# Kernel tuning notes

Measured on AMD Instinct MI355X. Metric: run time of the kernel, lower is better.

Reference implementation:

```python
import jax, jax.numpy as jnp
import numpy as np

H = 16      # num_heads
D = 1024    # input_dim
F = 4096    # feed_forward_hidden_size
B, S = 8, 4096
EPS = 1e-6


def _ln(x, g, b):
    mu = jnp.mean(x, axis=-1, keepdims=True)
    var = jnp.mean(jnp.square(x - mu), axis=-1, keepdims=True)
    return (x - mu) * jax.lax.rsqrt(var + EPS) * g + b


def _attn(Q, K, V):
    # per-head attention; original scales by sqrt(input_dim), NOT sqrt(head_dim)
    b, sq, d = Q.shape
    sk = K.shape[1]
    dh = d // H
    Qh = Q.reshape(b, sq, H, dh)
    Kh = K.reshape(b, sk, H, dh)
    Vh = V.reshape(b, sk, H, dh)
    scores = jnp.einsum('bqhd,bkhd->bhqk', Qh, Kh) / jnp.sqrt(jnp.float32(d))
    w = jax.nn.softmax(scores, axis=-1)
    return jnp.einsum('bhqk,bkhd->bqhd', w, Vh).reshape(b, sq, d)


def setup_inputs() -> dict:
    key = jax.random.key(0)
    ks = jax.random.split(key, 10)
    sc = 0.02
    np.random.seed(42)
    decode_input = jnp.asarray(np.random.random([B, 1, D]).astype(np.float32))
    return {
        'key': jax.random.normal(ks[0], (B, S, D), jnp.float32),
        'value': jax.random.normal(ks[1], (B, S, D), jnp.float32),
        'decode_input': decode_input,
        'Wq': jax.random.normal(ks[2], (D, D), jnp.float32) * sc,
        'bq': jnp.zeros((D,), jnp.float32),
        'Wk': jax.random.normal(ks[3], (D, D), jnp.float32) * sc,
        'bk': jnp.zeros((D,), jnp.float32),
        'Wv': jax.random.normal(ks[4], (D, D), jnp.float32) * sc,
        'bv': jnp.zeros((D,), jnp.float32),
        'Wo': jax.random.normal(ks[5], (D, D), jnp.float32) * sc,
        'bo': jnp.zeros((D,), jnp.float32),
        'W1': jax.random.normal(ks[6], (D, F), jnp.float32) * sc,
        'b1': jnp.zeros((F,), jnp.float32),
        'W2': jax.random.normal(ks[7], (F, D), jnp.float32) * sc,
        'b2': jnp.zeros((D,), jnp.float32),
        'ln2_g': jnp.ones((D,), jnp.float32),
        'ln2_b': jnp.zeros((D,), jnp.float32),
        'lnf_g': jnp.ones((D,), jnp.float32),
        'lnf_b': jnp.zeros((D,), jnp.float32),
    }


def reference(key, value, decode_input, Wq, bq, Wk, bk, Wv, bv, Wo, bo,
              W1, b1, W2, b2, ln2_g, ln2_b, lnf_g, lnf_b):
    # K/V projections shared by both attention calls (original reuses mha_1)
    K = key @ Wk + bk            # [B,S,D]
    V = value @ Wv + bv          # [B,S,D]

    # mha_1: self-attention of decode_input would use its own K/V, but here
    # q=k=v=decode_input for the first call
    Q1 = decode_input @ Wq + bq
    K1 = decode_input @ Wk + bk
    V1 = decode_input @ Wv + bv
    mha1_out = _attn(Q1, K1, V1) @ Wo + bo   # [B,1,D]
    # note: layer_norm_mha_1 output is computed in original but never used

    # second call (original buggily calls mha_1 again): q=mha1_out (un-normed)
    Q2 = mha1_out @ Wq + bq
    mha2_out = _attn(Q2, K, V) @ Wo + bo     # [B,1,D]
    x = _ln(mha2_out + decode_input, ln2_g, ln2_b)

    ff = jax.nn.relu(x @ W1 + b1) @ W2 + b2
    return _ln(ff + x, lnf_g, lnf_b)
```

## Files before the change

### kernel.cpp

```cpp
#include <hip/hip_runtime.h>
#include <hip/hip_bf16.h>

#define NB 8
#define NS 4096
#define ND 1024
#define NH 16
#define NF 4096

typedef __attribute__((ext_vector_type(8))) short s16x8;
typedef __attribute__((ext_vector_type(4))) float f32x4;

__device__ __forceinline__ short f2bfs(float x) {
    __hip_bfloat16 h = __float2bfloat16(x);
    return *reinterpret_cast<short*>(&h);
}

__device__ __forceinline__ s16x8 pack8(float4 a, float4 b) {
    s16x8 r;
    r[0]=f2bfs(a.x); r[1]=f2bfs(a.y); r[2]=f2bfs(a.z); r[3]=f2bfs(a.w);
    r[4]=f2bfs(b.x); r[5]=f2bfs(b.y); r[6]=f2bfs(b.z); r[7]=f2bfs(b.w);
    return r;
}

template<int KC>
__global__ void __launch_bounds__(256) mvV_k(const float* __restrict__ x,
        const float* __restrict__ W, int K, int Cout, float* __restrict__ Pout)
{
    __shared__ float xs[KC * 8];
    int tid = threadIdx.x;
    int c = blockIdx.x * 256 + tid;
    int k0 = blockIdx.y * KC;
    for (int i = tid; i < KC * 8; i += 256) {
        int k = i >> 3, b = i & 7;
        xs[i] = x[(size_t)b * K + k0 + k];
    }
    __syncthreads();
    const float* Wp = W + (size_t)k0 * Cout + c;
    float acc[8] = {0,0,0,0,0,0,0,0};
    #pragma unroll 16
    for (int k = 0; k < KC; ++k) {
        float wv = Wp[(size_t)k * Cout];
        float4 x0 = *(const float4*)&xs[k * 8];
        float4 x1 = *(const float4*)&xs[k * 8 + 4];
        acc[0] += x0.x * wv; acc[1] += x0.y * wv; acc[2] += x0.z * wv; acc[3] += x0.w * wv;
        acc[4] += x1.x * wv; acc[5] += x1.y * wv; acc[6] += x1.z * wv; acc[7] += x1.w * wv;
    }
    float* op = Pout + ((size_t)blockIdx.y * 8) * Cout + c;
    #pragma unroll
    for (int b = 0; b < 8; ++b) op[(size_t)b * Cout] = acc[b];
}

template<int KC, int NP, int RELU>
__global__ void __launch_bounds__(256) mvP_k(const float* __restrict__ P,
        const float* __restrict__ bias, const float* __restrict__ W,
        int K, int Cout, float* __restrict__ Pout)
{
    __shared__ float xs[KC * 8];
    int tid = threadIdx.x;
    int c = blockIdx.x * 256 + tid;
    int k0 = blockIdx.y * KC;
    for (int i = tid; i < KC * 8; i += 256) {
        int b = i / KC, k = i % KC;
        float t = bias[k0 + k];
        #pragma unroll 8
        for (int p = 0; p < NP; ++p) t += P[((size_t)(p * 8 + b)) * K + k0 + k];
        if (RELU) t = fmaxf(t, 0.f);
        xs[k * 8 + b] = t;
    }
    __syncthreads();
    const float* Wp = W + (size_t)k0 * Cout + c;
    float acc[8] = {0,0,0,0,0,0,0,0};
    #pragma unroll 16
    for (int k = 0; k < KC; ++k) {
        float wv = Wp[(size_t)k * Cout];
        float4 x0 = *(const float4*)&xs[k * 8];
        float4 x1 = *(const float4*)&xs[k * 8 + 4];
        acc[0] += x0.x * wv; acc[1] += x0.y * wv; acc[2] += x0.z * wv; acc[3] += x0.w * wv;
        acc[4] += x1.x * wv; acc[5] += x1.y * wv; acc[6] += x1.z * wv; acc[7] += x1.w * wv;
    }
    float* op = Pout + ((size_t)blockIdx.y * 8) * Cout + c;
    #pragma unroll
    for (int b = 0; b < 8; ++b) op[(size_t)b * Cout] = acc[b];
}

template<int KC, int NCH>
__global__ void __launch_bounds__(256) mvH_k(const float* __restrict__ plp,
        const float* __restrict__ W, float* __restrict__ Pout)
{
    __shared__ float xs[4 * KC * 8];
    int tid = threadIdx.x, lane = tid & 63, wv = tid >> 6;
    int c = blockIdx.x * 256 + tid;
    int k0 = blockIdx.y * KC;
    int h = (blockIdx.x * 256 + wv * 64) >> 6;
    for (int i = lane; i < 8 * KC; i += 64) {
        int b = i / KC, k = i % KC;
        float t = 0.f;
        #pragma unroll 8
        for (int ch = 0; ch < NCH; ++ch)
            t += plp[((size_t)((ch * 8 + b) * 16 + h)) * 1024 + k0 + k];
        xs[wv * 8 * KC + k * 8 + b] = t;
    }
    __syncthreads();
    const float* Wp = W + (size_t)k0 * 1024 + c;
    float acc[8] = {0,0,0,0,0,0,0,0};
    #pragma unroll 16
    for (int k = 0; k < KC; ++k) {
        float wvv = Wp[(size_t)k * 1024];
        float4 x0 = *(const float4*)&xs[wv * 8 * KC + k * 8];
        float4 x1 = *(const float4*)&xs[wv * 8 * KC + k * 8 + 4];
        acc[0] += x0.x * wvv; acc[1] += x0.y * wvv; acc[2] += x0.z * wvv; acc[3] += x0.w * wvv;
        acc[4] += x1.x * wvv; acc[5] += x1.y * wvv; acc[6] += x1.z * wvv; acc[7] += x1.w * wvv;
    }
    float* op = Pout + ((size_t)blockIdx.y * 8) * 1024 + c;
    #pragma unroll
    for (int b = 0; b < 8; ++b) op[(size_t)b * 1024] = acc[b];
}

__global__ void __launch_bounds__(256) u_k(const float* __restrict__ P,
        const float* __restrict__ bq, const float* __restrict__ Wk,
        unsigned short* __restrict__ u16)
{
    int bh = blockIdx.x;
    int b = bh >> 4, h = bh & 15;
    int lane = threadIdx.x & 63, wv = threadIdx.x >> 6;
    int cc = h * 64 + lane;
    float q = bq[cc];
    #pragma unroll 8
    for (int p = 0; p < 64; ++p) q += P[((size_t)(p * 8 + b)) * 1024 + cc];
    int dbase = blockIdx.y * 256;
    #pragma unroll 4
    for (int d = dbase + wv; d < dbase + 256; d += 4) {
        float v = Wk[(size_t)d * 1024 + cc] * q;
        for (int off = 32; off; off >>= 1) v += __shfl_down(v, off);
        if (lane == 0) u16[(size_t)bh * 1024 + d] = (unsigned short)f2bfs(v);
    }
}

__global__ void __launch_bounds__(256) scores_k(const float* __restrict__ key,
        const unsigned short* __restrict__ u16, float* __restrict__ sc)
{
    __shared__ __align__(16) unsigned short ul[16][1032];
    int b = blockIdx.x, tid = threadIdx.x;
    const uint4* src = (const uint4*)(u16 + (size_t)b * NH * 1024);
    for (int v = tid; v < 2048; v += 256) {
        int h = v >> 7, col = (v & 127) * 8;
        *(uint4*)&ul[h][col] = src[v];
    }
    __syncthreads();
    int lane = tid & 63, wv = tid >> 6;
    int r = lane & 15, g = lane >> 4;
    int s0 = blockIdx.y * 64 + wv * 16;
    const float* kp0 = key + ((size_t)(b * NS + s0 + r)) * ND + g * 8;
    f32x4 acc = {0.f, 0.f, 0.f, 0.f};
    float4 c0, c1, c2, c3, n0, n1, n2, n3;
    c0 = *(const float4*)(kp0);      c1 = *(const float4*)(kp0 + 4);
    c2 = *(const float4*)(kp0 + 32); c3 = *(const float4*)(kp0 + 36);
    #pragma unroll
    for (int k = 0; k < 1024; k += 64) {
        if (k + 64 < 1024) {
            const float* p = kp0 + k + 64;
            n0 = *(const float4*)(p);      n1 = *(const float4*)(p + 4);
            n2 = *(const float4*)(p + 32); n3 = *(const float4*)(p + 36);
        }
        s16x8 a0 = *(const s16x8*)&ul[r][k + g * 8];
        acc = __builtin_amdgcn_mfma_f32_16x16x32_bf16(a0, pack8(c0, c1), acc, 0, 0, 0);
        s16x8 a1 = *(const s16x8*)&ul[r][k + 32 + g * 8];
        acc = __builtin_amdgcn_mfma_f32_16x16x32_bf16(a1, pack8(c2, c3), acc, 0, 0, 0);
        c0 = n0; c1 = n1; c2 = n2; c3 = n3;
    }
    const float scl = 1.f / 32.f;
    #pragma unroll
    for (int j = 0; j < 4; ++j) {
        int h = g * 4 + j;
        sc[((size_t)(b * NH + h)) * NS + s0 + r] = acc[j] * scl;
    }
}

__global__ void __launch_bounds__(256) smred_k(const float* __restrict__ sc,
        float* __restrict__ minv)
{
    int bh = blockIdx.x, tid = threadIdx.x;
    const f32x4* row = (const f32x4*)(sc + (size_t)bh * NS);
    __shared__ float sd[4];
    f32x4 x0 = row[tid], x1 = row[256 + tid], x2 = row[512 + tid], x3 = row[768 + tid];
    float m = fmaxf(fmaxf(fmaxf(x0[0], x0[1]), fmaxf(x0[2], x0[3])),
                    fmaxf(fmaxf(x1[0], x1[1]), fmaxf(x1[2], x1[3])));
    m = fmaxf(m, fmaxf(fmaxf(fmaxf(x2[0], x2[1]), fmaxf(x2[2], x2[3])),
                       fmaxf(fmaxf(x3[0], x3[1]), fmaxf(x3[2], x3[3]))));
    for (int off = 32; off; off >>= 1) m = fmaxf(m, __shfl_down(m, off));
    if ((tid & 63) == 0) sd[tid >> 6] = m;
    __syncthreads();
    float mx = fmaxf(fmaxf(sd[0], sd[1]), fmaxf(sd[2], sd[3]));
    __syncthreads();
    float s = 0.f;
    #pragma unroll
    for (int j = 0; j < 4; ++j) s += __expf(x0[j] - mx) + __expf(x1[j] - mx)
                                   + __expf(x2[j] - mx) + __expf(x3[j] - mx);
    for (int off = 32; off; off >>= 1) s += __shfl_down(s, off);
    if ((tid & 63) == 0) sd[tid >> 6] = s;
    __syncthreads();
    if (tid == 0) {
        minv[bh * 2]     = mx;
        minv[bh * 2 + 1] = 1.f / (sd[0] + sd[1] + sd[2] + sd[3]);
    }
}

__global__ void __launch_bounds__(256) pool_k(const float* __restrict__ value,
        const float* __restrict__ scb, const float* __restrict__ minv,
        float* __restrict__ plp)
{
    __shared__ float pl[16][128];
    int b = blockIdx.x, sc4 = blockIdx.y, tid = threadIdx.x;
    int s0 = sc4 * 128;
    for (int i = tid; i < 2048; i += 256) {
        int h = i >> 7, si = i & 127;
        float mx  = minv[(b * 16 + h) * 2];
        float inv = minv[(b * 16 + h) * 2 + 1];
        pl[h][si] = __expf(scb[((size_t)(b * 16 + h)) * NS + s0 + si] - mx) * inv;
    }
    __syncthreads();
    const float* vp = value + ((size_t)(b * NS + s0)) * ND + tid * 4;
    f32x4 acc[16];
    #pragma unroll
    for (int h = 0; h < 16; ++h) acc[h] = (f32x4){0.f, 0.f, 0.f, 0.f};
    f32x4 v0,v1,v2,v3,v4,v5,v6,v7;
    v0 = *(const f32x4*)(vp + 0*ND); v1 = *(const f32x4*)(vp + 1*ND);
    v2 = *(const f32x4*)(vp + 2*ND); v3 = *(const f32x4*)(vp + 3*ND);
    v4 = *(const f32x4*)(vp + 4*ND); v5 = *(const f32x4*)(vp + 5*ND);
    v6 = *(const f32x4*)(vp + 6*ND); v7 = *(const f32x4*)(vp + 7*ND);
    for (int g = 0; g < 128; g += 8) {
        f32x4 n0,n1,n2,n3,n4,n5,n6,n7;
        if (g + 8 < 128) {
            const float* p = vp + (size_t)(g + 8) * ND;
            n0 = *(const f32x4*)(p + 0*ND); n1 = *(const f32x4*)(p + 1*ND);
            n2 = *(const f32x4*)(p + 2*ND); n3 = *(const f32x4*)(p + 3*ND);
            n4 = *(const f32x4*)(p + 4*ND); n5 = *(const f32x4*)(p + 5*ND);
            n6 = *(const f32x4*)(p + 6*ND); n7 = *(const f32x4*)(p + 7*ND);
        }
        #pragma unroll
        for (int h = 0; h < 16; ++h) {
            f32x4 wa = *(const f32x4*)&pl[h][g];
            f32x4 wb = *(const f32x4*)&pl[h][g + 4];
            acc[h] += v0 * wa[0] + v1 * wa[1] + v2 * wa[2] + v3 * wa[3]
                    + v4 * wb[0] + v5 * wb[1] + v6 * wb[2] + v7 * wb[3];
        }
        v0 = n0; v1 = n1; v2 = n2; v3 = n3;
        v4 = n4; v5 = n5; v6 = n6; v7 = n7;
    }
    float* o = plp + ((size_t)((sc4 * 8 + b) * 16)) * 1024 + tid * 4;
    #pragma unroll
    for (int h = 0; h < 16; ++h) *(f32x4*)(o + (size_t)h * 1024) = acc[h];
}

__global__ void __launch_bounds__(256) lnp_k(const float* __restrict__ P, int np,
        const float* __restrict__ bias, const float* __restrict__ add,
        const float* __restrict__ g, const float* __restrict__ be,
        float* __restrict__ out)
{
    int b = blockIdx.x, tid = threadIdx.x;
    __shared__ float sd[4];
    int c = tid * 4;
    f32x4 t = *(const f32x4*)&bias[c];
    t += *(const f32x4*)&add[(size_t)b * 1024 + c];
    #pragma unroll 8
    for (int p = 0; p < np; ++p)
        t += *(const f32x4*)&P[((size_t)(p * 8 + b)) * 1024 + c];
    float loc = t[0] + t[1] + t[2] + t[3];
    for (int off = 32; off; off >>= 1) loc += __shfl_down(loc, off);
    if ((tid & 63) == 0) sd[tid >> 6] = loc;
    __syncthreads();
    float mu = (sd[0] + sd[1] + sd[2] + sd[3]) * (1.f / 1024.f);
    __syncthreads();
    f32x4 d = t - mu;
    float v = d[0]*d[0] + d[1]*d[1] + d[2]*d[2] + d[3]*d[3];
    for (int off = 32; off; off >>= 1) v += __shfl_down(v, off);
    if ((tid & 63) == 0) sd[tid >> 6] = v;
    __syncthreads();
    float var = (sd[0] + sd[1] + sd[2] + sd[3]) * (1.f / 1024.f);
    float rs = rsqrtf(var + 1e-6f);
    f32x4 gg = *(const f32x4*)&g[c];
    f32x4 bb = *(const f32x4*)&be[c];
    f32x4 o = d * rs * gg + bb;
    *(f32x4*)&out[(size_t)b * 1024 + c] = o;
}

extern "C" void kernel_launch(void* const* d_in, const int* in_sizes, int n_in,
                              void* d_out, int out_size, void* d_ws, size_t ws_size,
                              hipStream_t stream)
{
    const float* key   = (const float*)d_in[0];
    const float* value = (const float*)d_in[1];
    const float* dec   = (const float*)d_in[2];
    const float* Wq = (const float*)d_in[3];  const float* bq = (const float*)d_in[4];
    const float* Wk = (const float*)d_in[5];
    const float* Wv = (const float*)d_in[7];  const float* bv = (const float*)d_in[8];
    const float* Wo = (const float*)d_in[9];  const float* bo = (const float*)d_in[10];
    const float* W1 = (const float*)d_in[11]; const float* b1 = (const float*)d_in[12];
    const float* W2 = (const float*)d_in[13]; const float* b2 = (const float*)d_in[14];
    const float* g2 = (const float*)d_in[15]; const float* be2 = (const float*)d_in[16];
    const float* gf = (const float*)d_in[17]; const float* bef = (const float*)d_in[18];

    float* ws = (float*)d_ws;
    float* scb  = ws;
    float* plp  = scb  + 524288;
    float* P1   = plp  + 4194304;
    float* P2   = P1   + 524288;
    float* Pff1 = P2   + 524288;
    float* Pff2 = Pff1 + 524288;
    float* xbuf = Pff2 + 524288;
    float* minv = xbuf + 8192;
    unsigned short* u16 = (unsigned short*)(minv + 256);

    dim3 blk(256);

    mvV_k<16><<<dim3(4,64), blk, 0, stream>>>(dec, Wv, 1024, 1024, P1);
    mvP_k<16,64,0><<<dim3(4,64), blk, 0, stream>>>(P1, bv, Wo, 1024, 1024, P2);
    mvP_k<16,64,0><<<dim3(4,64), blk, 0, stream>>>(P2, bo, Wq, 1024, 1024, P1);

    u_k<<<dim3(128,4), blk, 0, stream>>>(P1, bq, Wk, u16);

    scores_k<<<dim3(8,64), blk, 0, stream>>>(key, u16, scb);
    smred_k<<<dim3(128), blk, 0, stream>>>(scb, minv);
    pool_k<<<dim3(8,32), blk, 0, stream>>>(value, scb, minv, plp);

    mvH_k<16,32><<<dim3(4,64), blk, 0, stream>>>(plp, Wv, P2);
    mvP_k<16,64,0><<<dim3(4,64), blk, 0, stream>>>(P2, bv, Wo, 1024, 1024, P1);
    lnp_k<<<dim3(8), blk, 0, stream>>>(P1, 64, bo, dec, g2, be2, xbuf);

    mvV_k<64><<<dim3(16,16), blk, 0, stream>>>(xbuf, W1, 1024, 4096, Pff1);
    mvP_k<64,16,1><<<dim3(4,64), blk, 0, stream>>>(Pff1, b1, W2, 4096, 1024, Pff2);
    lnp_k<<<dim3(8), blk, 0, stream>>>(Pff2, 64, b2, xbuf, gf, bef, (float*)d_out);

    (void)in_sizes; (void)n_in; (void)out_size; (void)ws_size;
}
```

Measured before the change: 180.9 us.

## Fuse post-attention tail into one cooperative persistent kernel with grid syncs

```diff
diff --git a/kernel.cpp b/kernel.cpp
--- a/kernel.cpp
+++ b/kernel.cpp
@@ -1,5 +1,8 @@
 #include <hip/hip_runtime.h>
 #include <hip/hip_bf16.h>
+#include <hip/hip_cooperative_groups.h>
+
+namespace cg = cooperative_groups;
 
 #define NB 8
 #define NS 4096
@@ -21,6 +24,13 @@
     r[4]=f2bfs(b.x); r[5]=f2bfs(b.y); r[6]=f2bfs(b.z); r[7]=f2bfs(b.w);
     return r;
 }
+
+__device__ __forceinline__ void gsync(cg::grid_group& g) {
+    __threadfence();
+    g.sync();
+    __threadfence();
+}
+
 
 template<int KC>
 __global__ void __launch_bounds__(256) mvV_k(const float* __restrict__ x,
@@ -81,39 +91,6 @@
     float* op = Pout + ((size_t)blockIdx.y * 8) * Cout + c;
     #pragma unroll
     for (int b = 0; b < 8; ++b) op[(size_t)b * Cout] = acc[b];
-}
-
-template<int KC, int NCH>
-__global__ void __launch_bounds__(256) mvH_k(const float* __restrict__ plp,
-        const float* __restrict__ W, float* __restrict__ Pout)
-{
-    __shared__ float xs[4 * KC * 8];
-    int tid = threadIdx.x, lane = tid & 63, wv = tid >> 6;
-    int c = blockIdx.x * 256 + tid;
-    int k0 = blockIdx.y * KC;
-    int h = (blockIdx.x * 256 + wv * 64) >> 6;
-    for (int i = lane; i < 8 * KC; i += 64) {
-        int b = i / KC, k = i % KC;
-        float t = 0.f;
-        #pragma unroll 8
-        for (int ch = 0; ch < NCH; ++ch)
-            t += plp[((size_t)((ch * 8 + b) * 16 + h)) * 1024 + k0 + k];
-        xs[wv * 8 * KC + k * 8 + b] = t;
-    }
-    __syncthreads();
-    const float* Wp = W + (size_t)k0 * 1024 + c;
-    float acc[8] = {0,0,0,0,0,0,0,0};
-    #pragma unroll 16
-    for (int k = 0; k < KC; ++k) {
-        float wvv = Wp[(size_t)k * 1024];
-        float4 x0 = *(const float4*)&xs[wv * 8 * KC + k * 8];
-        float4 x1 = *(const float4*)&xs[wv * 8 * KC + k * 8 + 4];
-        acc[0] += x0.x * wvv; acc[1] += x0.y * wvv; acc[2] += x0.z * wvv; acc[3] += x0.w * wvv;
-        acc[4] += x1.x * wvv; acc[5] += x1.y * wvv; acc[6] += x1.z * wvv; acc[7] += x1.w * wvv;
-    }
-    float* op = Pout + ((size_t)blockIdx.y * 8) * 1024 + c;
-    #pragma unroll
-    for (int b = 0; b < 8; ++b) op[(size_t)b * 1024] = acc[b];
 }
 
 __global__ void __launch_bounds__(256) u_k(const float* __restrict__ P,
@@ -252,36 +229,233 @@
     for (int h = 0; h < 16; ++h) *(f32x4*)(o + (size_t)h * 1024) = acc[h];
 }
 
-__global__ void __launch_bounds__(256) lnp_k(const float* __restrict__ P, int np,
-        const float* __restrict__ bias, const float* __restrict__ add,
-        const float* __restrict__ g, const float* __restrict__ be,
-        float* __restrict__ out)
-{
-    int b = blockIdx.x, tid = threadIdx.x;
+__global__ void __launch_bounds__(256) coopB_k(
+        const float* __restrict__ plp, const float* __restrict__ Wv,
+        const float* __restrict__ bv, const float* __restrict__ Wo,
+        const float* __restrict__ bo, const float* __restrict__ dec,
+        const float* __restrict__ g2, const float* __restrict__ be2,
+        const float* __restrict__ W1, const float* __restrict__ b1,
+        const float* __restrict__ W2, const float* __restrict__ b2,
+        const float* __restrict__ gf, const float* __restrict__ bef,
+        float* __restrict__ Pd, float* __restrict__ Pe,
+        float* __restrict__ Pff1, float* __restrict__ Pff2,
+        float* __restrict__ xraw, float* __restrict__ xbuf,
+        float* __restrict__ ffraw, float* __restrict__ out)
+{
+    cg::grid_group grid = cg::this_grid();
+    __shared__ float sbuf[512];
     __shared__ float sd[4];
-    int c = tid * 4;
-    f32x4 t = *(const f32x4*)&bias[c];
-    t += *(const f32x4*)&add[(size_t)b * 1024 + c];
-    #pragma unroll 8
-    for (int p = 0; p < np; ++p)
-        t += *(const f32x4*)&P[((size_t)(p * 8 + b)) * 1024 + c];
-    float loc = t[0] + t[1] + t[2] + t[3];
-    for (int off = 32; off; off >>= 1) loc += __shfl_down(loc, off);
-    if ((tid & 63) == 0) sd[tid >> 6] = loc;
-    __syncthreads();
-    float mu = (sd[0] + sd[1] + sd[2] + sd[3]) * (1.f / 1024.f);
-    __syncthreads();
-    f32x4 d = t - mu;
-    float v = d[0]*d[0] + d[1]*d[1] + d[2]*d[2] + d[3]*d[3];
-    for (int off = 32; off; off >>= 1) v += __shfl_down(v, off);
-    if ((tid & 63) == 0) sd[tid >> 6] = v;
-    __syncthreads();
-    float var = (sd[0] + sd[1] + sd[2] + sd[3]) * (1.f / 1024.f);
-    float rs = rsqrtf(var + 1e-6f);
-    f32x4 gg = *(const f32x4*)&g[c];
-    f32x4 bb = *(const f32x4*)&be[c];
-    f32x4 o = d * rs * gg + bb;
-    *(f32x4*)&out[(size_t)b * 1024 + c] = o;
+    int tid = threadIdx.x, bid = blockIdx.x;
+
+    {
+        int cblk = bid & 3, kp = bid >> 2, k0 = kp * 16;
+        int wv = tid >> 6, lane = tid & 63;
+        int h = cblk * 4 + wv;
+        int c = cblk * 256 + tid;
+        int item = lane >> 1, chg = lane & 1;
+        int b = item >> 2, kv = item & 3;
+        const float* Pp = plp + ((size_t)(b * 16 + h)) * ND + k0 + kv * 4;
+        f32x4 v = {0,0,0,0};
+        #pragma unroll
+        for (int cc = 0; cc < 16; ++cc)
+            v += *(const f32x4*)(Pp + (size_t)(chg * 16 + cc) * 8 * 16 * ND);
+        v[0] += __shfl_down(v[0], 1); v[1] += __shfl_down(v[1], 1);
+        v[2] += __shfl_down(v[2], 1); v[3] += __shfl_down(v[3], 1);
+        if (chg == 0) {
+            #pragma unroll
+            for (int j = 0; j < 4; ++j) sbuf[wv * 128 + (kv * 4 + j) * 8 + b] = v[j];
+        }
+        __syncthreads();
+        {
+            const float* Wp = Wv + (size_t)k0 * 1024 + c;
+            const float* xs = &sbuf[wv * 128];
+            float acc[8] = {0,0,0,0,0,0,0,0};
+            #pragma unroll 16
+            for (int k = 0; k < 16; ++k) {
+                float wvv = Wp[(size_t)k * 1024];
+                float4 x0 = *(const float4*)&xs[k * 8];
+                float4 x1 = *(const float4*)&xs[k * 8 + 4];
+                acc[0] += x0.x * wvv; acc[1] += x0.y * wvv; acc[2] += x0.z * wvv; acc[3] += x0.w * wvv;
+                acc[4] += x1.x * wvv; acc[5] += x1.y * wvv; acc[6] += x1.z * wvv; acc[7] += x1.w * wvv;
+            }
+            float* op = Pd + ((size_t)kp * 8) * 1024 + c;
+            #pragma unroll
+            for (int b2_ = 0; b2_ < 8; ++b2_) op[(size_t)b2_ * 1024] = acc[b2_];
+        }
+    }
+    gsync(grid);
+
+    {
+        int cblk = bid & 3, kp = bid >> 2, k0 = kp * 16;
+        int c = cblk * 256 + tid;
+        {
+            int vec = tid >> 3, pg = tid & 7;
+            int b = vec >> 2, kv = vec & 3;
+            const float* Pp = Pd + (size_t)b * ND + k0 + kv * 4;
+            f32x4 v = {0,0,0,0};
+            #pragma unroll
+            for (int pp = 0; pp < 8; ++pp)
+                v += *(const f32x4*)(Pp + (size_t)(pg * 8 + pp) * 8 * ND);
+            #pragma unroll
+            for (int off = 4; off; off >>= 1) {
+                v[0] += __shfl_down(v[0], off); v[1] += __shfl_down(v[1], off);
+                v[2] += __shfl_down(v[2], off); v[3] += __shfl_down(v[3], off);
+            }
+            if (pg == 0) {
+                #pragma unroll
+                for (int j = 0; j < 4; ++j)
+                    sbuf[(kv * 4 + j) * 8 + b] = v[j] + bv[k0 + kv * 4 + j];
+            }
+        }
+        __syncthreads();
+        {
+            const float* Wp = Wo + (size_t)k0 * 1024 + c;
+            float acc[8] = {0,0,0,0,0,0,0,0};
+            #pragma unroll 16
+            for (int k = 0; k < 16; ++k) {
+                float wvv = Wp[(size_t)k * 1024];
+                float4 x0 = *(const float4*)&sbuf[k * 8];
+                float4 x1 = *(const float4*)&sbuf[k * 8 + 4];
+                acc[0] += x0.x * wvv; acc[1] += x0.y * wvv; acc[2] += x0.z * wvv; acc[3] += x0.w * wvv;
+                acc[4] += x1.x * wvv; acc[5] += x1.y * wvv; acc[6] += x1.z * wvv; acc[7] += x1.w * wvv;
+            }
+            float* op = Pe + ((size_t)kp * 8) * 1024 + c;
+            #pragma unroll
+            for (int b2_ = 0; b2_ < 8; ++b2_) op[(size_t)b2_ * 1024] = acc[b2_];
+        }
+    }
+    gsync(grid);
+
+    {
+        int b = bid >> 5, cbase = (bid & 31) * 32;
+        int ci = tid >> 3, pg = tid & 7;
+        float s = 0.f;
+        #pragma unroll
+        for (int pp = 0; pp < 8; ++pp)
+            s += Pe[((size_t)((pg * 8 + pp) * 8 + b)) * ND + cbase + ci];
+        for (int off = 4; off; off >>= 1) s += __shfl_down(s, off);
+        if (pg == 0)
+            xraw[(size_t)b * ND + cbase + ci] = s + bo[cbase + ci] + dec[(size_t)b * ND + cbase + ci];
+    }
+    gsync(grid);
+
+    if (bid < 8) {
+        int c = tid * 4;
+        f32x4 t = *(const f32x4*)&xraw[(size_t)bid * ND + c];
+        float loc = t[0] + t[1] + t[2] + t[3];
+        for (int off = 32; off; off >>= 1) loc += __shfl_down(loc, off);
+        if ((tid & 63) == 0) sd[tid >> 6] = loc;
+        __syncthreads();
+        float mu = (sd[0] + sd[1] + sd[2] + sd[3]) * (1.f / 1024.f);
+        __syncthreads();
+        f32x4 d = t - mu;
+        float v = d[0]*d[0] + d[1]*d[1] + d[2]*d[2] + d[3]*d[3];
+        for (int off = 32; off; off >>= 1) v += __shfl_down(v, off);
+        if ((tid & 63) == 0) sd[tid >> 6] = v;
+        __syncthreads();
+        float var = (sd[0] + sd[1] + sd[2] + sd[3]) * (1.f / 1024.f);
+        float rs = rsqrtf(var + 1e-6f);
+        f32x4 gg = *(const f32x4*)&g2[c];
+        f32x4 bb = *(const f32x4*)&be2[c];
+        f32x4 o = d * rs * gg + bb;
+        *(f32x4*)&xbuf[(size_t)bid * ND + c] = o;
+    }
+    gsync(grid);
+
+    {
+        int cblk = bid & 15, kp = bid >> 4, k0 = kp * 64;
+        int c = cblk * 256 + tid;
+        for (int i = tid; i < 512; i += 256) {
+            int k = i >> 3, b = i & 7;
+            sbuf[i] = xbuf[(size_t)b * ND + k0 + k];
+        }
+        __syncthreads();
+        const float* Wp = W1 + (size_t)k0 * 4096 + c;
+        float acc[8] = {0,0,0,0,0,0,0,0};
+        #pragma unroll 16
+        for (int k = 0; k < 64; ++k) {
+            float wvv = Wp[(size_t)k * 4096];
+            float4 x0 = *(const float4*)&sbuf[k * 8];
+            float4 x1 = *(const float4*)&sbuf[k * 8 + 4];
+            acc[0] += x0.x * wvv; acc[1] += x0.y * wvv; acc[2] += x0.z * wvv; acc[3] += x0.w * wvv;
+            acc[4] += x1.x * wvv; acc[5] += x1.y * wvv; acc[6] += x1.z * wvv; acc[7] += x1.w * wvv;
+        }
+        float* op = Pff1 + ((size_t)kp * 8) * 4096 + c;
+        #pragma unroll
+        for (int b2_ = 0; b2_ < 8; ++b2_) op[(size_t)b2_ * 4096] = acc[b2_];
+    }
+    gsync(grid);
+
+    {
+        int cblk = bid & 3, kp = bid >> 2, k0 = kp * 64;
+        int c = cblk * 256 + tid;
+        {
+            int vec = tid >> 1, pg = tid & 1;
+            int b = vec >> 4, kv = vec & 15;
+            const float* Pp = Pff1 + (size_t)b * NF + k0 + kv * 4;
+            f32x4 v = {0,0,0,0};
+            #pragma unroll
+            for (int pp = 0; pp < 8; ++pp)
+                v += *(const f32x4*)(Pp + (size_t)(pg * 8 + pp) * 8 * NF);
+            v[0] += __shfl_down(v[0], 1); v[1] += __shfl_down(v[1], 1);
+            v[2] += __shfl_down(v[2], 1); v[3] += __shfl_down(v[3], 1);
+            if (pg == 0) {
+                #pragma unroll
+                for (int j = 0; j < 4; ++j)
+                    sbuf[(kv * 4 + j) * 8 + b] = fmaxf(v[j] + b1[k0 + kv * 4 + j], 0.f);
+            }
+        }
+        __syncthreads();
+        const float* Wp = W2 + (size_t)k0 * 1024 + c;
+        float acc[8] = {0,0,0,0,0,0,0,0};
+        #pragma unroll 16
+        for (int k = 0; k < 64; ++k) {
+            float wvv = Wp[(size_t)k * 1024];
+            float4 x0 = *(const float4*)&sbuf[k * 8];
+            float4 x1 = *(const float4*)&sbuf[k * 8 + 4];
+            acc[0] += x0.x * wvv; acc[1] += x0.y * wvv; acc[2] += x0.z * wvv; acc[3] += x0.w * wvv;
+            acc[4] += x1.x * wvv; acc[5] += x1.y * wvv; acc[6] += x1.z * wvv; acc[7] += x1.w * wvv;
+        }
+        float* op = Pff2 + ((size_t)kp * 8) * 1024 + c;
+        #pragma unroll
+        for (int b2_ = 0; b2_ < 8; ++b2_) op[(size_t)b2_ * 1024] = acc[b2_];
+    }
+    gsync(grid);
+
+    {
+        int b = bid >> 5, cbase = (bid & 31) * 32;
+        int ci = tid >> 3, pg = tid & 7;
+        float s = 0.f;
+        #pragma unroll
+        for (int pp = 0; pp < 8; ++pp)
+            s += Pff2[((size_t)((pg * 8 + pp) * 8 + b)) * ND + cbase + ci];
+        for (int off = 4; off; off >>= 1) s += __shfl_down(s, off);
+        if (pg == 0)
+            ffraw[(size_t)b * ND + cbase + ci] = s + b2[cbase + ci] + xbuf[(size_t)b * ND + cbase + ci];
+    }
+    gsync(grid);
+
+    if (bid < 8) {
+        int c = tid * 4;
+        f32x4 t = *(const f32x4*)&ffraw[(size_t)bid * ND + c];
+        float loc = t[0] + t[1] + t[2] + t[3];
+        for (int off = 32; off; off >>= 1) loc += __shfl_down(loc, off);
+        if ((tid & 63) == 0) sd[tid >> 6] = loc;
+        __syncthreads();
+        float mu = (sd[0] + sd[1] + sd[2] + sd[3]) * (1.f / 1024.f);
+        __syncthreads();
+        f32x4 d = t - mu;
+        float v = d[0]*d[0] + d[1]*d[1] + d[2]*d[2] + d[3]*d[3];
+        for (int off = 32; off; off >>= 1) v += __shfl_down(v, off);
+        if ((tid & 63) == 0) sd[tid >> 6] = v;
+        __syncthreads();
+        float var = (sd[0] + sd[1] + sd[2] + sd[3]) * (1.f / 1024.f);
+        float rs = rsqrtf(var + 1e-6f);
+        f32x4 gg = *(const f32x4*)&gf[c];
+        f32x4 bb = *(const f32x4*)&bef[c];
+        f32x4 o = d * rs * gg + bb;
+        *(f32x4*)&out[(size_t)bid * ND + c] = o;
+    }
 }
 
 extern "C" void kernel_launch(void* const* d_in, const int* in_sizes, int n_in,
@@ -301,35 +475,43 @@
     const float* gf = (const float*)d_in[17]; const float* bef = (const float*)d_in[18];
 
     float* ws = (float*)d_ws;
-    float* scb  = ws;
+    float* Pa   = ws;
+    float* Pb   = Pa   + 524288;
+    float* Pq   = Pb   + 524288;
+    float* scb  = Pq   + 524288;
     float* plp  = scb  + 524288;
-    float* P1   = plp  + 4194304;
-    float* P2   = P1   + 524288;
-    float* Pff1 = P2   + 524288;
+    float* Pd   = plp  + 4194304;
+    float* Pe   = Pd   + 524288;
+    float* Pff1 = Pe   + 524288;
     float* Pff2 = Pff1 + 524288;
-    float* xbuf = Pff2 + 524288;
-    float* minv = xbuf + 8192;
+    float* xraw = Pff2 + 524288;
+    float* xbuf = xraw + 8192;
+    float* ffraw= xbuf + 8192;
+    float* minv = ffraw+ 8192;
     unsigned short* u16 = (unsigned short*)(minv + 256);
+    float* outp = (float*)d_out;
 
     dim3 blk(256);
 
-    mvV_k<16><<<dim3(4,64), blk, 0, stream>>>(dec, Wv, 1024, 1024, P1);
-    mvP_k<16,64,0><<<dim3(4,64), blk, 0, stream>>>(P1, bv, Wo, 1024, 1024, P2);
-    mvP_k<16,64,0><<<dim3(4,64), blk, 0, stream>>>(P2, bo, Wq, 1024, 1024, P1);
-
-    u_k<<<dim3(128,4), blk, 0, stream>>>(P1, bq, Wk, u16);
+    mvV_k<16><<<dim3(4,64), blk, 0, stream>>>(dec, Wv, 1024, 1024, Pa);
+    mvP_k<16,64,0><<<dim3(4,64), blk, 0, stream>>>(Pa, bv, Wo, 1024, 1024, Pb);
+    mvP_k<16,64,0><<<dim3(4,64), blk, 0, stream>>>(Pb, bo, Wq, 1024, 1024, Pq);
+    u_k<<<dim3(128,4), blk, 0, stream>>>(Pq, bq, Wk, u16);
 
     scores_k<<<dim3(8,64), blk, 0, stream>>>(key, u16, scb);
     smred_k<<<dim3(128), blk, 0, stream>>>(scb, minv);
     pool_k<<<dim3(8,32), blk, 0, stream>>>(value, scb, minv, plp);
 
-    mvH_k<16,32><<<dim3(4,64), blk, 0, stream>>>(plp, Wv, P2);
-    mvP_k<16,64,0><<<dim3(4,64), blk, 0, stream>>>(P2, bv, Wo, 1024, 1024, P1);
-    lnp_k<<<dim3(8), blk, 0, stream>>>(P1, 64, bo, dec, g2, be2, xbuf);
-
-    mvV_k<64><<<dim3(16,16), blk, 0, stream>>>(xbuf, W1, 1024, 4096, Pff1);
-    mvP_k<64,16,1><<<dim3(4,64), blk, 0, stream>>>(Pff1, b1, W2, 4096, 1024, Pff2);
-    lnp_k<<<dim3(8), blk, 0, stream>>>(Pff2, 64, b2, xbuf, gf, bef, (float*)d_out);
+    {
+        void* args[] = { (void*)&plp, (void*)&Wv, (void*)&bv, (void*)&Wo, (void*)&bo,
+                         (void*)&dec, (void*)&g2, (void*)&be2,
+                         (void*)&W1, (void*)&b1, (void*)&W2, (void*)&b2,
+                         (void*)&gf, (void*)&bef,
+                         (void*)&Pd, (void*)&Pe, (void*)&Pff1, (void*)&Pff2,
+                         (void*)&xraw, (void*)&xbuf, (void*)&ffraw, (void*)&outp };
+        hipLaunchCooperativeKernel((const void*)coopB_k, dim3(256), dim3(256),
+                                   args, 0, stream);
+    }
 
     (void)in_sizes; (void)n_in; (void)out_size; (void)ws_size;
 }
```

Result: slower. 667.7 us (+269.2%).

## Fuse attention scores, exp and value pooling into one kernel with deferred normalization

Applied to the files above, without the earlier changes.

```diff
diff --git a/kernel.cpp b/kernel.cpp
--- a/kernel.cpp
+++ b/kernel.cpp
@@ -21,6 +21,7 @@
     r[4]=f2bfs(b.x); r[5]=f2bfs(b.y); r[6]=f2bfs(b.z); r[7]=f2bfs(b.w);
     return r;
 }
+
 
 template<int KC>
 __global__ void __launch_bounds__(256) mvV_k(const float* __restrict__ x,
@@ -81,39 +82,6 @@
     float* op = Pout + ((size_t)blockIdx.y * 8) * Cout + c;
     #pragma unroll
     for (int b = 0; b < 8; ++b) op[(size_t)b * Cout] = acc[b];
-}
-
-template<int KC, int NCH>
-__global__ void __launch_bounds__(256) mvH_k(const float* __restrict__ plp,
-        const float* __restrict__ W, float* __restrict__ Pout)
-{
-    __shared__ float xs[4 * KC * 8];
-    int tid = threadIdx.x, lane = tid & 63, wv = tid >> 6;
-    int c = blockIdx.x * 256 + tid;
-    int k0 = blockIdx.y * KC;
-    int h = (blockIdx.x * 256 + wv * 64) >> 6;
-    for (int i = lane; i < 8 * KC; i += 64) {
-        int b = i / KC, k = i % KC;
-        float t = 0.f;
-        #pragma unroll 8
-        for (int ch = 0; ch < NCH; ++ch)
-            t += plp[((size_t)((ch * 8 + b) * 16 + h)) * 1024 + k0 + k];
-        xs[wv * 8 * KC + k * 8 + b] = t;
-    }
-    __syncthreads();
-    const float* Wp = W + (size_t)k0 * 1024 + c;
-    float acc[8] = {0,0,0,0,0,0,0,0};
-    #pragma unroll 16
-    for (int k = 0; k < KC; ++k) {
-        float wvv = Wp[(size_t)k * 1024];
-        float4 x0 = *(const float4*)&xs[wv * 8 * KC + k * 8];
-        float4 x1 = *(const float4*)&xs[wv * 8 * KC + k * 8 + 4];
-        acc[0] += x0.x * wvv; acc[1] += x0.y * wvv; acc[2] += x0.z * wvv; acc[3] += x0.w * wvv;
-        acc[4] += x1.x * wvv; acc[5] += x1.y * wvv; acc[6] += x1.z * wvv; acc[7] += x1.w * wvv;
-    }
-    float* op = Pout + ((size_t)blockIdx.y * 8) * 1024 + c;
-    #pragma unroll
-    for (int b = 0; b < 8; ++b) op[(size_t)b * 1024] = acc[b];
 }
 
 __global__ void __launch_bounds__(256) u_k(const float* __restrict__ P,
@@ -136,122 +104,6 @@
     }
 }
 
-__global__ void __launch_bounds__(256) scores_k(const float* __restrict__ key,
-        const unsigned short* __restrict__ u16, float* __restrict__ sc)
-{
-    __shared__ __align__(16) unsigned short ul[16][1032];
-    int b = blockIdx.x, tid = threadIdx.x;
-    const uint4* src = (const uint4*)(u16 + (size_t)b * NH * 1024);
-    for (int v = tid; v < 2048; v += 256) {
-        int h = v >> 7, col = (v & 127) * 8;
-        *(uint4*)&ul[h][col] = src[v];
-    }
-    __syncthreads();
-    int lane = tid & 63, wv = tid >> 6;
-    int r = lane & 15, g = lane >> 4;
-    int s0 = blockIdx.y * 64 + wv * 16;
-    const float* kp0 = key + ((size_t)(b * NS + s0 + r)) * ND + g * 8;
-    f32x4 acc = {0.f, 0.f, 0.f, 0.f};
-    float4 c0, c1, c2, c3, n0, n1, n2, n3;
-    c0 = *(const float4*)(kp0);      c1 = *(const float4*)(kp0 + 4);
-    c2 = *(const float4*)(kp0 + 32); c3 = *(const float4*)(kp0 + 36);
-    #pragma unroll
-    for (int k = 0; k < 1024; k += 64) {
-        if (k + 64 < 1024) {
-            const float* p = kp0 + k + 64;
-            n0 = *(const float4*)(p);      n1 = *(const float4*)(p + 4);
-            n2 = *(const float4*)(p + 32); n3 = *(const float4*)(p + 36);
-        }
-        s16x8 a0 = *(const s16x8*)&ul[r][k + g * 8];
-        acc = __builtin_amdgcn_mfma_f32_16x16x32_bf16(a0, pack8(c0, c1), acc, 0, 0, 0);
-        s16x8 a1 = *(const s16x8*)&ul[r][k + 32 + g * 8];
-        acc = __builtin_amdgcn_mfma_f32_16x16x32_bf16(a1, pack8(c2, c3), acc, 0, 0, 0);
-        c0 = n0; c1 = n1; c2 = n2; c3 = n3;
-    }
-    const float scl = 1.f / 32.f;
-    #pragma unroll
-    for (int j = 0; j < 4; ++j) {
-        int h = g * 4 + j;
-        sc[((size_t)(b * NH + h)) * NS + s0 + r] = acc[j] * scl;
-    }
-}
-
-__global__ void __launch_bounds__(256) smred_k(const float* __restrict__ sc,
-        float* __restrict__ minv)
-{
-    int bh = blockIdx.x, tid = threadIdx.x;
-    const f32x4* row = (const f32x4*)(sc + (size_t)bh * NS);
-    __shared__ float sd[4];
-    f32x4 x0 = row[tid], x1 = row[256 + tid], x2 = row[512 + tid], x3 = row[768 + tid];
-    float m = fmaxf(fmaxf(fmaxf(x0[0], x0[1]), fmaxf(x0[2], x0[3])),
-                    fmaxf(fmaxf(x1[0], x1[1]), fmaxf(x1[2], x1[3])));
-    m = fmaxf(m, fmaxf(fmaxf(fmaxf(x2[0], x2[1]), fmaxf(x2[2], x2[3])),
-                       fmaxf(fmaxf(x3[0], x3[1]), fmaxf(x3[2], x3[3]))));
-    for (int off = 32; off; off >>= 1) m = fmaxf(m, __shfl_down(m, off));
-    if ((tid & 63) == 0) sd[tid >> 6] = m;
-    __syncthreads();
-    float mx = fmaxf(fmaxf(sd[0], sd[1]), fmaxf(sd[2], sd[3]));
-    __syncthreads();
-    float s = 0.f;
-    #pragma unroll
-    for (int j = 0; j < 4; ++j) s += __expf(x0[j] - mx) + __expf(x1[j] - mx)
-                                   + __expf(x2[j] - mx) + __expf(x3[j] - mx);
-    for (int off = 32; off; off >>= 1) s += __shfl_down(s, off);
-    if ((tid & 63) == 0) sd[tid >> 6] = s;
-    __syncthreads();
-    if (tid == 0) {
-        minv[bh * 2]     = mx;
-        minv[bh * 2 + 1] = 1.f / (sd[0] + sd[1] + sd[2] + sd[3]);
-    }
-}
-
-__global__ void __launch_bounds__(256) pool_k(const float* __restrict__ value,
-        const float* __restrict__ scb, const float* __restrict__ minv,
-        float* __restrict__ plp)
-{
-    __shared__ float pl[16][128];
-    int b = blockIdx.x, sc4 = blockIdx.y, tid = threadIdx.x;
-    int s0 = sc4 * 128;
-    for (int i = tid; i < 2048; i += 256) {
-        int h = i >> 7, si = i & 127;
-        float mx  = minv[(b * 16 + h) * 2];
-        float inv = minv[(b * 16 + h) * 2 + 1];
-        pl[h][si] = __expf(scb[((size_t)(b * 16 + h)) * NS + s0 + si] - mx) * inv;
-    }
-    __syncthreads();
-    const float* vp = value + ((size_t)(b * NS + s0)) * ND + tid * 4;
-    f32x4 acc[16];
-    #pragma unroll
-    for (int h = 0; h < 16; ++h) acc[h] = (f32x4){0.f, 0.f, 0.f, 0.f};
-    f32x4 v0,v1,v2,v3,v4,v5,v6,v7;
-    v0 = *(const f32x4*)(vp + 0*ND); v1 = *(const f32x4*)(vp + 1*ND);
-    v2 = *(const f32x4*)(vp + 2*ND); v3 = *(const f32x4*)(vp + 3*ND);
-    v4 = *(const f32x4*)(vp + 4*ND); v5 = *(const f32x4*)(vp + 5*ND);
-    v6 = *(const f32x4*)(vp + 6*ND); v7 = *(const f32x4*)(vp + 7*ND);
-    for (int g = 0; g < 128; g += 8) {
-        f32x4 n0,n1,n2,n3,n4,n5,n6,n7;
-        if (g + 8 < 128) {
-            const float* p = vp + (size_t)(g + 8) * ND;
-            n0 = *(const f32x4*)(p + 0*ND); n1 = *(const f32x4*)(p + 1*ND);
-            n2 = *(const f32x4*)(p + 2*ND); n3 = *(const f32x4*)(p + 3*ND);
-            n4 = *(const f32x4*)(p + 4*ND); n5 = *(const f32x4*)(p + 5*ND);
-            n6 = *(const f32x4*)(p + 6*ND); n7 = *(const f32x4*)(p + 7*ND);
-        }
-        #pragma unroll
-        for (int h = 0; h < 16; ++h) {
-            f32x4 wa = *(const f32x4*)&pl[h][g];
-            f32x4 wb = *(const f32x4*)&pl[h][g + 4];
-            acc[h] += v0 * wa[0] + v1 * wa[1] + v2 * wa[2] + v3 * wa[3]
-                    + v4 * wb[0] + v5 * wb[1] + v6 * wb[2] + v7 * wb[3];
-        }
-        v0 = n0; v1 = n1; v2 = n2; v3 = n3;
-        v4 = n4; v5 = n5; v6 = n6; v7 = n7;
-    }
-    float* o = plp + ((size_t)((sc4 * 8 + b) * 16)) * 1024 + tid * 4;
-    #pragma unroll
-    for (int h = 0; h < 16; ++h) *(f32x4*)(o + (size_t)h * 1024) = acc[h];
-}
-
 __global__ void __launch_bounds__(256) lnp_k(const float* __restrict__ P, int np,
         const float* __restrict__ bias, const float* __restrict__ add,
         const float* __restrict__ g, const float* __restrict__ be,
@@ -284,6 +136,135 @@
     *(f32x4*)&out[(size_t)b * 1024 + c] = o;
 }
 
+__global__ void __launch_bounds__(256) attn_k(const float* __restrict__ key,
+        const float* __restrict__ value, const unsigned short* __restrict__ u16,
+        float* __restrict__ plp, float* __restrict__ dnm)
+{
+    __shared__ __align__(16) unsigned short ul[16][1032];
+    __shared__ float pl[16][64];
+    int b = blockIdx.x, ch = blockIdx.y, tid = threadIdx.x;
+    int s0 = ch * 64;
+
+    const uint4* src = (const uint4*)(u16 + (size_t)b * NH * 1024);
+    for (int v = tid; v < 2048; v += 256) {
+        int h = v >> 7, col = (v & 127) * 8;
+        *(uint4*)&ul[h][col] = src[v];
+    }
+    __syncthreads();
+
+    {
+        int lane = tid & 63, wv = tid >> 6;
+        int r = lane & 15, g = lane >> 4;
+        const float* kp0 = key + ((size_t)(b * NS + s0 + wv * 16 + r)) * ND + g * 8;
+        f32x4 acc = {0.f, 0.f, 0.f, 0.f};
+        float4 c0, c1, c2, c3, n0, n1, n2, n3;
+        c0 = *(const float4*)(kp0);      c1 = *(const float4*)(kp0 + 4);
+        c2 = *(const float4*)(kp0 + 32); c3 = *(const float4*)(kp0 + 36);
+        #pragma unroll
+        for (int k = 0; k < 1024; k += 64) {
+            if (k + 64 < 1024) {
+                const float* p = kp0 + k + 64;
+                n0 = *(const float4*)(p);      n1 = *(const float4*)(p + 4);
+                n2 = *(const float4*)(p + 32); n3 = *(const float4*)(p + 36);
+            }
+            s16x8 a0 = *(const s16x8*)&ul[r][k + g * 8];
+            acc = __builtin_amdgcn_mfma_f32_16x16x32_bf16(a0, pack8(c0, c1), acc, 0, 0, 0);
+            s16x8 a1 = *(const s16x8*)&ul[r][k + 32 + g * 8];
+            acc = __builtin_amdgcn_mfma_f32_16x16x32_bf16(a1, pack8(c2, c3), acc, 0, 0, 0);
+            c0 = n0; c1 = n1; c2 = n2; c3 = n3;
+        }
+        const float scl = 1.f / 32.f;
+        #pragma unroll
+        for (int j = 0; j < 4; ++j) {
+            int h = g * 4 + j;
+            pl[h][wv * 16 + r] = __expf(acc[j] * scl);
+        }
+    }
+    __syncthreads();
+
+    if (tid < 16) {
+        float s = 0.f;
+        #pragma unroll 16
+        for (int si = 0; si < 64; ++si) s += pl[tid][si];
+        dnm[((size_t)(ch * 8 + b)) * 16 + tid] = s;
+    }
+
+    {
+        const float* vp = value + ((size_t)(b * NS + s0)) * ND + tid * 4;
+        f32x4 acc[16];
+        #pragma unroll
+        for (int h = 0; h < 16; ++h) acc[h] = (f32x4){0.f, 0.f, 0.f, 0.f};
+        f32x4 v0,v1,v2,v3,v4,v5,v6,v7;
+        v0 = *(const f32x4*)(vp + 0*ND); v1 = *(const f32x4*)(vp + 1*ND);
+        v2 = *(const f32x4*)(vp + 2*ND); v3 = *(const f32x4*)(vp + 3*ND);
+        v4 = *(const f32x4*)(vp + 4*ND); v5 = *(const f32x4*)(vp + 5*ND);
+        v6 = *(const f32x4*)(vp + 6*ND); v7 = *(const f32x4*)(vp + 7*ND);
+        for (int g = 0; g < 64; g += 8) {
+            f32x4 n0,n1,n2,n3,n4,n5,n6,n7;
+            if (g + 8 < 64) {
+                const float* p = vp + (size_t)(g + 8) * ND;
+                n0 = *(const f32x4*)(p + 0*ND); n1 = *(const f32x4*)(p + 1*ND);
+                n2 = *(const f32x4*)(p + 2*ND); n3 = *(const f32x4*)(p + 3*ND);
+                n4 = *(const f32x4*)(p + 4*ND); n5 = *(const f32x4*)(p + 5*ND);
+                n6 = *(const f32x4*)(p + 6*ND); n7 = *(const f32x4*)(p + 7*ND);
+            }
+            #pragma unroll
+            for (int h = 0; h < 16; ++h) {
+                f32x4 wa = *(const f32x4*)&pl[h][g];
+                f32x4 wb = *(const f32x4*)&pl[h][g + 4];
+                acc[h] += v0 * wa[0] + v1 * wa[1] + v2 * wa[2] + v3 * wa[3]
+                        + v4 * wb[0] + v5 * wb[1] + v6 * wb[2] + v7 * wb[3];
+            }
+            v0 = n0; v1 = n1; v2 = n2; v3 = n3;
+            v4 = n4; v5 = n5; v6 = n6; v7 = n7;
+        }
+        float* o = plp + ((size_t)((ch * 8 + b) * 16)) * 1024 + tid * 4;
+        #pragma unroll
+        for (int h = 0; h < 16; ++h) *(f32x4*)(o + (size_t)h * 1024) = acc[h];
+    }
+}
+
+template<int KC, int NCH>
+__global__ void __launch_bounds__(256) mvH_k(const float* __restrict__ plp,
+        const float* __restrict__ dnm, const float* __restrict__ W,
+        float* __restrict__ Pout)
+{
+    __shared__ float xs[4 * KC * 8];
+    int tid = threadIdx.x, lane = tid & 63, wv = tid >> 6;
+    int c = blockIdx.x * 256 + tid;
+    int k0 = blockIdx.y * KC;
+    int h = blockIdx.x * 4 + wv;
+    float den = 0.f;
+    if (lane < 8) {
+        #pragma unroll 8
+        for (int ch = 0; ch < NCH; ++ch)
+            den += dnm[((size_t)(ch * 8 + lane)) * 16 + h];
+    }
+    float inv8 = (lane < 8) ? 1.f / den : 0.f;
+    for (int i = lane; i < 8 * KC; i += 64) {
+        int b = i / KC, k = i % KC;
+        float t = 0.f;
+        #pragma unroll 8
+        for (int ch = 0; ch < NCH; ++ch)
+            t += plp[((size_t)((ch * 8 + b) * 16 + h)) * 1024 + k0 + k];
+        xs[wv * 8 * KC + k * 8 + b] = t * __shfl(inv8, b);
+    }
+    __syncthreads();
+    const float* Wp = W + (size_t)k0 * 1024 + c;
+    float acc[8] = {0,0,0,0,0,0,0,0};
+    #pragma unroll 16
+    for (int k = 0; k < KC; ++k) {
+        float wvv = Wp[(size_t)k * 1024];
+        float4 x0 = *(const float4*)&xs[wv * 8 * KC + k * 8];
+        float4 x1 = *(const float4*)&xs[wv * 8 * KC + k * 8 + 4];
+        acc[0] += x0.x * wvv; acc[1] += x0.y * wvv; acc[2] += x0.z * wvv; acc[3] += x0.w * wvv;
+        acc[4] += x1.x * wvv; acc[5] += x1.y * wvv; acc[6] += x1.z * wvv; acc[7] += x1.w * wvv;
+    }
+    float* op = Pout + ((size_t)blockIdx.y * 8) * 1024 + c;
+    #pragma unroll
+    for (int b = 0; b < 8; ++b) op[(size_t)b * 1024] = acc[b];
+}
+
 extern "C" void kernel_launch(void* const* d_in, const int* in_sizes, int n_in,
                               void* d_out, int out_size, void* d_ws, size_t ws_size,
                               hipStream_t stream)
@@ -301,35 +282,35 @@
     const float* gf = (const float*)d_in[17]; const float* bef = (const float*)d_in[18];
 
     float* ws = (float*)d_ws;
-    float* scb  = ws;
-    float* plp  = scb  + 524288;
-    float* P1   = plp  + 4194304;
-    float* P2   = P1   + 524288;
-    float* Pff1 = P2   + 524288;
+    float* Pa   = ws;
+    float* Pb   = Pa   + 524288;
+    float* Pq   = Pb   + 524288;
+    float* plp  = Pq   + 524288;
+    float* dnm  = plp  + 8388608;
+    float* Pd   = dnm  + 8192;
+    float* Pe   = Pd   + 524288;
+    float* Pff1 = Pe   + 524288;
     float* Pff2 = Pff1 + 524288;
     float* xbuf = Pff2 + 524288;
-    float* minv = xbuf + 8192;
-    unsigned short* u16 = (unsigned short*)(minv + 256);
+    unsigned short* u16 = (unsigned short*)(xbuf + 8192);
+    float* outp = (float*)d_out;
 
     dim3 blk(256);
 
-    mvV_k<16><<<dim3(4,64), blk, 0, stream>>>(dec, Wv, 1024, 1024, P1);
-    mvP_k<16,64,0><<<dim3(4,64), blk, 0, stream>>>(P1, bv, Wo, 1024, 1024, P2);
-    mvP_k<16,64,0><<<dim3(4,64), blk, 0, stream>>>(P2, bo, Wq, 1024, 1024, P1);
-
-    u_k<<<dim3(128,4), blk, 0, stream>>>(P1, bq, Wk, u16);
-
-    scores_k<<<dim3(8,64), blk, 0, stream>>>(key, u16, scb);
-    smred_k<<<dim3(128), blk, 0, stream>>>(scb, minv);
-    pool_k<<<dim3(8,32), blk, 0, stream>>>(value, scb, minv, plp);
-
-    mvH_k<16,32><<<dim3(4,64), blk, 0, stream>>>(plp, Wv, P2);
-    mvP_k<16,64,0><<<dim3(4,64), blk, 0, stream>>>(P2, bv, Wo, 1024, 1024, P1);
-    lnp_k<<<dim3(8), blk, 0, stream>>>(P1, 64, bo, dec, g2, be2, xbuf);
+    mvV_k<16><<<dim3(4,64), blk, 0, stream>>>(dec, Wv, 1024, 1024, Pa);
+    mvP_k<16,64,0><<<dim3(4,64), blk, 0, stream>>>(Pa, bv, Wo, 1024, 1024, Pb);
+    mvP_k<16,64,0><<<dim3(4,64), blk, 0, stream>>>(Pb, bo, Wq, 1024, 1024, Pq);
+    u_k<<<dim3(128,4), blk, 0, stream>>>(Pq, bq, Wk, u16);
+
+    attn_k<<<dim3(8,64), blk, 0, stream>>>(key, value, u16, plp, dnm);
+
+    mvH_k<16,64><<<dim3(4,64), blk, 0, stream>>>(plp, dnm, Wv, Pd);
+    mvP_k<16,64,0><<<dim3(4,64), blk, 0, stream>>>(Pd, bv, Wo, 1024, 1024, Pe);
+    lnp_k<<<dim3(8), blk, 0, stream>>>(Pe, 64, bo, dec, g2, be2, xbuf);
 
     mvV_k<64><<<dim3(16,16), blk, 0, stream>>>(xbuf, W1, 1024, 4096, Pff1);
     mvP_k<64,16,1><<<dim3(4,64), blk, 0, stream>>>(Pff1, b1, W2, 4096, 1024, Pff2);
-    lnp_k<<<dim3(8), blk, 0, stream>>>(Pff2, 64, b2, xbuf, gf, bef, (float*)d_out);
+    lnp_k<<<dim3(8), blk, 0, stream>>>(Pff2, 64, b2, xbuf, gf, bef, outp);
 
     (void)in_sizes; (void)n_in; (void)out_size; (void)ws_size;
 }
```

New measurement: 178.7 us. About the same (-1.2%).
